# Optimization experiments

Hardware: AMD Instinct MI355X
Metric: run time of the kernel (lower is better)

Reference implementation:

```python
import jax, jax.numpy as jnp
import numpy as np

N_NODES = 100_000
N_EDGES = 1_600_000
N_GRAPHS = 64
EPS = 1e-7  # GENConv message epsilon
D_IN, D_H, D_OUT, OUT_DIM = 128, 192, 128, 10


def _w(k, fan_in, fan_out):
    return jax.random.normal(k, (fan_in, fan_out), jnp.float32) * (1.0 / np.sqrt(fan_in))


def setup_inputs() -> dict:
    key = jax.random.key(0)
    ks = jax.random.split(key, 8)
    return {
        "x": jax.random.normal(ks[0], (N_NODES, D_IN), jnp.float32),
        "W0": _w(ks[1], D_IN, D_H), "b0": jnp.zeros((D_H,), jnp.float32),
        "W1": _w(ks[2], D_H, D_H), "b1": jnp.zeros((D_H,), jnp.float32),
        "W2": _w(ks[3], D_H, D_H), "b2": jnp.zeros((D_H,), jnp.float32),
        "W3": _w(ks[4], D_H, D_OUT), "b3": jnp.zeros((D_OUT,), jnp.float32),
        "Wfc": _w(ks[5], D_OUT, OUT_DIM), "bfc": jnp.zeros((OUT_DIM,), jnp.float32),
        "edge_index": jax.random.randint(ks[6], (2, N_EDGES), 0, N_NODES, jnp.int32),
        "batch": jnp.sort(jax.random.randint(ks[7], (N_NODES,), 0, N_GRAPHS, jnp.int32)),
    }


def _genconv(x, W, b, src, dst):
    # GENConv (num_layers=1, aggr='add'): message = relu(x_j) + eps,
    # scatter-add to dst, residual add, single Linear MLP.
    msg = jax.nn.relu(x[src]) + EPS          # [E, d]
    agg = jax.ops.segment_sum(msg, dst, num_segments=N_NODES)  # [N, d]
    return (x + agg) @ W + b


def reference(x, W0, b0, W1, b1, W2, b2, W3, b3, Wfc, bfc, edge_index, batch):
    src, dst = edge_index[0], edge_index[1]  # source_to_target flow
    for W, b in ((W0, b0), (W1, b1), (W2, b2), (W3, b3)):
        x = _genconv(x, W, b, src, dst)
    # global mean pool over graphs
    sums = jax.ops.segment_sum(x, batch, num_segments=N_GRAPHS)
    counts = jax.ops.segment_sum(jnp.ones((x.shape[0],), x.dtype), batch,
                                 num_segments=N_GRAPHS)
    pooled = sums / jnp.maximum(counts, 1.0)[:, None]  # [G, D_OUT]
    logits = pooled @ Wfc + bfc                        # [G, OUT_DIM]
    return jax.nn.log_softmax(logits, axis=1)
```

## Files before the change

### kernel.cpp

```cpp
#include <hip/hip_runtime.h>
#include <hip/hip_bf16.h>
#include <stdint.h>

constexpr int NN = 100000;
constexpr int NE = 1600000;
constexpr int NG = 64;
constexpr int S  = 192;
constexpr int NB_SCAN = 98;
constexpr unsigned int ZOFF = (unsigned int)NN * 384u;

constexpr int PREP_INDEG_BLK = 1563;
constexpr int PREP_CONVX_BLK = 12500;
constexpr int PREP_CONVW_BLK = 384;
constexpr int PREP_GB_BLK    = 391;
constexpr int PREP_GRID = PREP_INDEG_BLK + PREP_CONVX_BLK + PREP_CONVW_BLK + PREP_GB_BLK;

constexpr int EG_BLOCKS = 391;
constexpr int HROW = 50048;
constexpr int QROW = HROW / 4;

typedef __bf16 bf16x8 __attribute__((ext_vector_type(8)));
typedef float  f32x16 __attribute__((ext_vector_type(16)));
typedef float  f32x2  __attribute__((ext_vector_type(2)));

union U16x4 { uint4 u; bf16x8 b; };

__device__ __forceinline__ float bl(unsigned int u) { return __uint_as_float(u << 16); }
__device__ __forceinline__ float bh(unsigned int u) { return __uint_as_float(u & 0xffff0000u); }
__device__ __forceinline__ float b16f(unsigned short u) { return __uint_as_float(((unsigned int)u) << 16); }
__device__ __forceinline__ unsigned int fb(float f) {
    unsigned int u = __float_as_uint(f);
    return (u + 0x7fffu + ((u >> 16) & 1u)) >> 16;
}
__device__ __forceinline__ unsigned int prelu(unsigned int u) {
    unsigned int r;
    asm("v_pk_max_f16 %0, %1, %2" : "=v"(r) : "v"(u), "v"(0u));
    return r;
}
__device__ __forceinline__ unsigned int cnt2bf(unsigned int h) {
    float f0 = (float)(h & 0xffffu);
    float f1 = (float)(h >> 16);
    return (__float_as_uint(f0) >> 16) | (__float_as_uint(f1) & 0xffff0000u);
}

__global__ __launch_bounds__(256) void k_prep(const float* __restrict__ x,
                                              const int* __restrict__ ei,
                                              const int* __restrict__ bat,
                                              const float* __restrict__ W0, const float* __restrict__ W1,
                                              const float* __restrict__ W2,
                                              unsigned short* __restrict__ A_,
                                              int* __restrict__ indeg, int* __restrict__ slot,
                                              unsigned short* __restrict__ T0, unsigned short* __restrict__ T1,
                                              unsigned short* __restrict__ T2,
                                              int* __restrict__ nstart) {
    const int b = blockIdx.x;
    if (b < PREP_INDEG_BLK) {
        int e4 = (b * 256 + threadIdx.x) * 4;
        if (e4 < NE) {
            int4 d = *(const int4*)(ei + NE + e4);
            int4 sl;
            sl.x = atomicAdd(&indeg[d.x], 1);
            sl.y = atomicAdd(&indeg[d.y], 1);
            sl.z = atomicAdd(&indeg[d.z], 1);
            sl.w = atomicAdd(&indeg[d.w], 1);
            *(int4*)(slot + e4) = sl;
        }
    } else if (b < PREP_INDEG_BLK + PREP_CONVX_BLK) {
        int id = (b - PREP_INDEG_BLK) * 256 + threadIdx.x;
        if (id < 96) ((unsigned int*)(A_ + (size_t)NN * S))[id] = 0u;
        int row = id >> 5, c4 = id & 31;
        float4 v = ((const float4*)x)[id];
        uint2 a;
        a.x = fb(v.x) | (fb(v.y) << 16);
        a.y = fb(v.z) | (fb(v.w) << 16);
        *(uint2*)(A_ + row * S + c4 * 4) = a;
    } else if (b < PREP_INDEG_BLK + PREP_CONVX_BLK + PREP_CONVW_BLK) {
        int id = (b - PREP_INDEG_BLK - PREP_CONVX_BLK) * 256 + threadIdx.x;
        const float* W; unsigned short* T; int N, base;
        if      (id < 24576) { W = W0; T = T0; N = 192; base = 0;     }
        else if (id < 61440) { W = W1; T = T1; N = 192; base = 24576; }
        else                 { W = W2; T = T2; N = 192; base = 61440; }
        int lid = id - base;
        int ci = lid >> 3, j = lid & 7;
        int kc = ci / N, n = ci % N;
        T[lid] = (unsigned short)fb(W[(kc * 8 + j) * N + n]);
    } else {
        int n = (b - PREP_INDEG_BLK - PREP_CONVX_BLK - PREP_CONVW_BLK) * 256 + threadIdx.x;
        if (n < NN) {
            int b0 = bat[n];
            int bprev = (n == 0) ? -1 : bat[n - 1];
            for (int g = bprev + 1; g <= b0; g++) nstart[g] = n;
            if (n == NN - 1)
                for (int g = b0 + 1; g < NG; g++) nstart[g] = NN;
        }
    }
}

__global__ __launch_bounds__(1024) void k_scan1(const int* __restrict__ indeg, int* __restrict__ offs,
                                                int* __restrict__ partials) {
    __shared__ int s[1024];
    int t = threadIdx.x;
    int gid = blockIdx.x * 1024 + t;
    int v = (gid < NN) ? indeg[gid] : 0;
    s[t] = v;
    __syncthreads();
    for (int d = 1; d < 1024; d <<= 1) {
        int tv = (t >= d) ? s[t - d] : 0;
        __syncthreads();
        s[t] += tv;
        __syncthreads();
    }
    if (gid < NN) offs[gid + 1] = s[t];
    if (t == 1023) partials[blockIdx.x] = s[1023];
}

__device__ __forceinline__ int toff(const int* __restrict__ offs, const int* __restrict__ part, int j) {
    return j ? (offs[j] + part[(j - 1) >> 10]) : 0;
}

__global__ __launch_bounds__(256) void k_fill(const int* __restrict__ ei, const int* __restrict__ offs,
                                              const int* __restrict__ praw,
                                              const int* __restrict__ slot, int* __restrict__ csr,
                                              int* __restrict__ part2) {
    __shared__ int s[128];
    __shared__ int spx[128];
    const int t = threadIdx.x;
    int v = 0;
    if (t < 128) {
        v = (t < NB_SCAN) ? praw[t] : 0;
        s[t] = v;
    }
    __syncthreads();
    for (int d = 1; d < 128; d <<= 1) {
        int tv = (t < 128 && t >= d) ? s[t - d] : 0;
        __syncthreads();
        if (t < 128) s[t] += tv;
        __syncthreads();
    }
    if (t < 128) spx[t] = s[t] - v;
    __syncthreads();
    if (blockIdx.x == 0 && t < NB_SCAN) part2[t] = spx[t];

    int e4 = (blockIdx.x * 256 + t) * 4;
    if (e4 >= NE) return;
    int4 sv = *(const int4*)(ei + e4);
    int4 dv = *(const int4*)(ei + NE + e4);
    int4 sl = *(const int4*)(slot + e4);
    csr[(dv.x ? offs[dv.x] + spx[(dv.x - 1) >> 10] : 0) + sl.x] = sv.x;
    csr[(dv.y ? offs[dv.y] + spx[(dv.y - 1) >> 10] : 0) + sl.y] = sv.y;
    csr[(dv.z ? offs[dv.z] + spx[(dv.z - 1) >> 10] : 0) + sl.z] = sv.z;
    csr[(dv.w ? offs[dv.w] + spx[(dv.w - 1) >> 10] : 0) + sl.w] = sv.w;
}

__global__ __launch_bounds__(256, 8) void k_agg192(const unsigned short* __restrict__ Ain,
                                                   unsigned short* __restrict__ Yout,
                                                   const int* __restrict__ offs,
                                                   const int* __restrict__ part,
                                                   const int* __restrict__ indeg,
                                                   const int* __restrict__ csr) {
    const int w = threadIdx.x >> 6, lane = threadIdx.x & 63;
    const int i = __builtin_amdgcn_readfirstlane(blockIdx.x * 4 + w);
    const bool act = lane < 48;
    const int deg   = __builtin_amdgcn_readfirstlane(indeg[i]);
    const int start = __builtin_amdgcn_readfirstlane(toff(offs, part, i));
    const int fo = (act ? lane : 47) * 8;
    const char* Ab = (const char*)Ain;

    f32x2 A01, A23;
    {
        uint2 p = *(const uint2*)(Ab + (size_t)i * 384 + fo);
        const float ed = 1e-7f * (float)deg;
        A01 = (f32x2){bl(p.x) + ed, bh(p.x) + ed};
        A23 = (f32x2){bl(p.y) + ed, bh(p.y) + ed};
    }

    const int* ecsr = csr + start;
    for (int e = 0; e < deg; e += 16) {
        unsigned int off[16];
#pragma unroll
        for (int k = 0; k < 16; k++) {
            int v = ecsr[e + k];
            off[k] = (e + k < deg) ? (unsigned int)v * 384u : ZOFF;
        }
        uint2 p[16];
#pragma unroll
        for (int k = 0; k < 16; k++)
            p[k] = *(const uint2*)(Ab + (size_t)off[k] + fo);
#pragma unroll
        for (int k = 0; k < 16; k++) {
            unsigned int rx = prelu(p[k].x), ry = prelu(p[k].y);
            A01 += (f32x2){bl(rx), bh(rx)};
            A23 += (f32x2){bl(ry), bh(ry)};
        }
    }
    if (act) {
        uint2 o;
        o.x = fb(A01.x) | (fb(A01.y) << 16);
        o.y = fb(A23.x) | (fb(A23.y) << 16);
        *(uint2*)(Yout + (size_t)i * S + lane * 4) = o;
    }
}

__global__ __launch_bounds__(256, 8) void k_agg128(const unsigned short* __restrict__ Ain,
                                                   unsigned short* __restrict__ Yout,
                                                   const int* __restrict__ offs,
                                                   const int* __restrict__ part,
                                                   const int* __restrict__ indeg,
                                                   const int* __restrict__ csr) {
    const int w = threadIdx.x >> 6, lane = threadIdx.x & 63;
    const int i = __builtin_amdgcn_readfirstlane(blockIdx.x * 4 + w);
    const int deg   = __builtin_amdgcn_readfirstlane(indeg[i]);
    const int start = __builtin_amdgcn_readfirstlane(toff(offs, part, i));
    const int fo = lane * 4;
    const char* Ab = (const char*)Ain;

    f32x2 A01;
    {
        unsigned int p = *(const unsigned int*)(Ab + (size_t)i * 384 + fo);
        const float ed = 1e-7f * (float)deg;
        A01 = (f32x2){bl(p) + ed, bh(p) + ed};
    }

    const int* ecsr = csr + start;
    for (int e = 0; e < deg; e += 16) {
        unsigned int off[16];
#pragma unroll
        for (int k = 0; k < 16; k++) {
            int v = ecsr[e + k];
            off[k] = (e + k < deg) ? (unsigned int)v * 384u : ZOFF;
        }
        unsigned int q[16];
#pragma unroll
        for (int k = 0; k < 16; k++)
            q[k] = *(const unsigned int*)(Ab + (size_t)off[k] + fo);
#pragma unroll
        for (int k = 0; k < 16; k++) {
            unsigned int r = prelu(q[k]);
            A01 += (f32x2){bl(r), bh(r)};
        }
    }
    *(unsigned int*)(Yout + (size_t)i * S + lane * 2) =
        fb(A01.x) | (fb(A01.y) << 16);
}

template <int K, int N>
__global__ __launch_bounds__(256) void k_gemm(const unsigned short* __restrict__ Yin,
                                              const unsigned short* __restrict__ WtC,
                                              const float* __restrict__ bias,
                                              unsigned short* __restrict__ Aout) {
    static_assert(K % 16 == 0 && N % 32 == 0, "");
    const int w = threadIdx.x >> 6, lane = threadIdx.x & 63;
    const int rt = blockIdx.x * 4 + w;
    if (rt >= (NN / 32)) return;
    const int hl = lane >> 5, lr = lane & 31;
    const int row0 = rt * 32;
    f32x16 acc[N / 32];
#pragma unroll
    for (int c = 0; c < N / 32; c++)
#pragma unroll
        for (int r = 0; r < 16; r++) acc[c][r] = 0.f;

    const unsigned short* ap = Yin + (row0 + lr) * S + hl * 8;
    const uint4* b4 = (const uint4*)WtC;
#pragma unroll
    for (int ks = 0; ks < K / 16; ks++) {
        U16x4 a;
        a.u = *(const uint4*)(ap + ks * 16);
#pragma unroll
        for (int c = 0; c < N / 32; c++) {
            U16x4 b;
            b.u = b4[(ks * 2 + hl) * N + c * 32 + lr];
            acc[c] = __builtin_amdgcn_mfma_f32_32x32x16_bf16(a.b, b.b, acc[c], 0, 0, 0);
        }
    }
#pragma unroll
    for (int c = 0; c < N / 32; c++) {
        const int col = c * 32 + lr;
        const float bc = bias[col];
#pragma unroll
        for (int r = 0; r < 16; r++) {
            const int row = row0 + (r & 3) + 8 * (r >> 2) + 4 * hl;
            Aout[row * S + col] = (unsigned short)fb(acc[c][r] + bc);
        }
    }
}

__global__ __launch_bounds__(256) void k_histpool(const int* __restrict__ csr,
                                                  const int* __restrict__ offs,
                                                  const int* __restrict__ part,
                                                  const int* __restrict__ nstart,
                                                  unsigned int* __restrict__ hist,
                                                  const unsigned short* __restrict__ X3,
                                                  const int* __restrict__ bat,
                                                  const int* __restrict__ indeg,
                                                  float* __restrict__ sums, float* __restrict__ cnt,
                                                  float* __restrict__ degsum) {
    const int b = blockIdx.x;
    if (b < 256) {
        const int g = b >> 2, q = b & 3;
        unsigned int* hrow = hist + (size_t)g * HROW;
        const unsigned int q0 = q * QROW;
        for (int i = threadIdx.x; i < QROW; i += 256) hrow[q0 + i] = 0u;
        __syncthreads();
        const int s0 = toff(offs, part, nstart[g]);
        const int s1 = (g == NG - 1) ? NE : toff(offs, part, nstart[g + 1]);
        for (int p = s0 + threadIdx.x; p < s1; p += 256) {
            int src = csr[p];
            unsigned int h = (unsigned int)src >> 1;
            if (h - q0 < (unsigned int)QROW)
                atomicAdd(&hrow[h], 1u << (16 * (src & 1)));
        }
    } else {
        const int pb = b - 256;
        const int f = threadIdx.x;
        if (f >= 192) return;
        int n0 = pb * 50;
        int n1 = min(n0 + 50, NN);
        int cur = bat[n0];
        float acc = 0.f;
        int run = 0, dacc = 0;
        for (int n = n0; n < n1; n++) {
            int g = bat[n];
            if (g != cur) {
                atomicAdd(&sums[cur * 192 + f], acc);
                if (f == 0) { atomicAdd(&cnt[cur], (float)run); atomicAdd(&degsum[cur], (float)dacc); }
                acc = 0.f; run = 0; dacc = 0; cur = g;
            }
            acc += b16f(X3[(size_t)n * S + f]);
            run++;
            if (f == 0) dacc += indeg[n];
        }
        atomicAdd(&sums[cur * 192 + f], acc);
        if (f == 0) { atomicAdd(&cnt[cur], (float)run); atomicAdd(&degsum[cur], (float)dacc); }
    }
}

__global__ __launch_bounds__(384) void k_egemm(const unsigned short* __restrict__ X3,
                                               const unsigned int* __restrict__ hist,
                                               float* __restrict__ partials) {
    const int wv = threadIdx.x >> 6, lane = threadIdx.x & 63;
    const int b = blockIdx.x;
    const int j0 = b * 256;
    const int hl = lane >> 5, lr = lane & 31;
    const int feat = wv * 32 + lr;
    f32x16 acc[2];
#pragma unroll
    for (int m = 0; m < 2; m++)
#pragma unroll
        for (int r = 0; r < 16; r++) acc[m][r] = 0.f;

    for (int kk = 0; kk < 16; kk++) {
        const int jh = (j0 >> 1) + kk * 8 + hl * 4;
        U16x4 af[2];
#pragma unroll
        for (int m = 0; m < 2; m++) {
            uint4 h = *(const uint4*)(hist + (size_t)(m * 32 + lr) * HROW + jh);
            af[m].u = (uint4){cnt2bf(h.x), cnt2bf(h.y), cnt2bf(h.z), cnt2bf(h.w)};
        }
        U16x4 bf;
#pragma unroll
        for (int tp = 0; tp < 4; tp++) {
            int je = j0 + kk * 16 + hl * 8 + tp * 2;
            int ja = min(je, NN), jb = min(je + 1, NN);
            unsigned int u0 = X3[(size_t)ja * S + feat];
            unsigned int u1 = X3[(size_t)jb * S + feat];
            ((unsigned int*)&bf.u)[tp] = prelu(u0 | (u1 << 16));
        }
#pragma unroll
        for (int m = 0; m < 2; m++)
            acc[m] = __builtin_amdgcn_mfma_f32_32x32x16_bf16(af[m].b, bf.b, acc[m], 0, 0, 0);
    }
    float* pb = partials + (size_t)b * 12288;
#pragma unroll
    for (int m = 0; m < 2; m++)
#pragma unroll
        for (int r = 0; r < 16; r++) {
            const int g = m * 32 + (r & 3) + 8 * (r >> 2) + 4 * hl;
            pb[g * 192 + feat] = acc[m][r];
        }
}

__global__ __launch_bounds__(192) void k_head(const float* __restrict__ sums,
                                              const float* __restrict__ partials,
                                              const float* __restrict__ cnt, const float* __restrict__ degsum,
                                              const float* __restrict__ W3, const float* __restrict__ b3,
                                              const float* __restrict__ Wfc, const float* __restrict__ bfc,
                                              float* __restrict__ out) {
    __shared__ float py[192];
    __shared__ float tl[128];
    __shared__ float lg[10];
    const int g = blockIdx.x, t = threadIdx.x;
    const float inv = 1.f / fmaxf(cnt[g], 1.f);
    const float ed = 1e-7f * degsum[g];
    const float* pp = partials + g * 192 + t;
    float s0 = 0.f, s1 = 0.f, s2 = 0.f, s3 = 0.f;
    int p = 0;
    for (; p + 4 <= EG_BLOCKS; p += 4) {
        s0 += pp[(size_t)(p + 0) * 12288];
        s1 += pp[(size_t)(p + 1) * 12288];
        s2 += pp[(size_t)(p + 2) * 12288];
        s3 += pp[(size_t)(p + 3) * 12288];
    }
    for (; p < EG_BLOCKS; p++) s0 += pp[(size_t)p * 12288];
    py[t] = (sums[g * 192 + t] + ((s0 + s1) + (s2 + s3)) + ed) * inv;
    __syncthreads();
    if (t < 128) {
        float tf = b3[t];
        for (int k = 0; k < 192; k++) tf += py[k] * W3[k * 128 + t];
        tl[t] = tf;
    }
    __syncthreads();
    if (t < 10) {
        float sf = bfc[t];
        for (int f = 0; f < 128; f++) sf += tl[f] * Wfc[f * 10 + t];
        lg[t] = sf;
    }
    __syncthreads();
    if (t < 10) {
        float m = lg[0];
        for (int k = 1; k < 10; k++) m = fmaxf(m, lg[k]);
        float se = 0.f;
        for (int k = 0; k < 10; k++) se += expf(lg[k] - m);
        out[g * 10 + t] = lg[t] - m - logf(se);
    }
}

constexpr size_t A0_OFF     = 0;
constexpr size_t A1_OFF     = 38400384;
constexpr size_t HIST_REL   = 0;
constexpr size_t PARTS_REL  = 12812288;
constexpr size_t CSR_OFF    = 76800384;
constexpr size_t OFFS_OFF   = 83200384;
constexpr size_t INDEG_OFF  = 83600512;
constexpr size_t SUMS_OFF   = 84000512;
constexpr size_t CNT_OFF    = 84049664;
constexpr size_t DEGS_OFF   = 84049920;
constexpr size_t PART_OFF   = 84050176;
constexpr size_t PART2_OFF  = 84050688;
constexpr size_t NSTART_OFF = 84051200;
constexpr size_t WT0_OFF    = 84051456;
constexpr size_t WT1_OFF    = 84100608;
constexpr size_t WT2_OFF    = 84174336;

extern "C" void kernel_launch(void* const* d_in, const int* in_sizes, int n_in,
                              void* d_out, int out_size, void* d_ws, size_t ws_size,
                              hipStream_t stream) {
    const float* x   = (const float*)d_in[0];
    const float* W0  = (const float*)d_in[1];
    const float* b0  = (const float*)d_in[2];
    const float* W1  = (const float*)d_in[3];
    const float* b1  = (const float*)d_in[4];
    const float* W2  = (const float*)d_in[5];
    const float* b2  = (const float*)d_in[6];
    const float* W3  = (const float*)d_in[7];
    const float* b3  = (const float*)d_in[8];
    const float* Wfc = (const float*)d_in[9];
    const float* bfc = (const float*)d_in[10];
    const int*   ei  = (const int*)d_in[11];
    const int*   bat = (const int*)d_in[12];
    float* out = (float*)d_out;

    char* ws = (char*)d_ws;
    unsigned short* A0  = (unsigned short*)(ws + A0_OFF);
    unsigned short* A1  = (unsigned short*)(ws + A1_OFF);
    int* slot   = (int*)(ws + A1_OFF);
    unsigned int* hist  = (unsigned int*)(ws + A1_OFF + HIST_REL);
    float* parts        = (float*)(ws + A1_OFF + PARTS_REL);
    int* csr    = (int*)(ws + CSR_OFF);
    int* offs   = (int*)(ws + OFFS_OFF);
    int* indeg  = (int*)(ws + INDEG_OFF);
    int* part   = (int*)(ws + PART_OFF);
    int* part2  = (int*)(ws + PART2_OFF);
    int* nstart = (int*)(ws + NSTART_OFF);
    unsigned short* Wt0 = (unsigned short*)(ws + WT0_OFF);
    unsigned short* Wt1 = (unsigned short*)(ws + WT1_OFF);
    unsigned short* Wt2 = (unsigned short*)(ws + WT2_OFF);
    float* sums   = (float*)(ws + SUMS_OFF);
    float* cnt    = (float*)(ws + CNT_OFF);
    float* degsum = (float*)(ws + DEGS_OFF);

    hipMemsetAsync(ws + INDEG_OFF, 0, 449664, stream);

    k_prep<<<PREP_GRID, 256, 0, stream>>>(x, ei, bat, W0, W1, W2, A0, indeg, slot,
                                          Wt0, Wt1, Wt2, nstart);

    k_scan1<<<NB_SCAN, 1024, 0, stream>>>(indeg, offs, part);
    k_fill<<<(NE / 4 + 255) / 256, 256, 0, stream>>>(ei, offs, part, slot, csr, part2);

    const int AGG_GRID  = NN / 4;
    const int GEMM_GRID = (NN / 32 + 3) / 4;

    k_agg128<<<AGG_GRID, 256, 0, stream>>>(A0, A1, offs, part2, indeg, csr);
    k_gemm<128, 192><<<GEMM_GRID, 256, 0, stream>>>(A1, Wt0, b0, A0);
    k_agg192<<<AGG_GRID, 256, 0, stream>>>(A0, A1, offs, part2, indeg, csr);
    k_gemm<192, 192><<<GEMM_GRID, 256, 0, stream>>>(A1, Wt1, b1, A0);
    k_agg192<<<AGG_GRID, 256, 0, stream>>>(A0, A1, offs, part2, indeg, csr);
    k_gemm<192, 192><<<GEMM_GRID, 256, 0, stream>>>(A1, Wt2, b2, A0);

    k_histpool<<<2256, 256, 0, stream>>>(csr, offs, part2, nstart, hist, A0, bat, indeg,
                                         sums, cnt, degsum);
    k_egemm<<<EG_BLOCKS, 384, 0, stream>>>(A0, hist, parts);
    k_head<<<NG, 192, 0, stream>>>(sums, parts, cnt, degsum, W3, b3, Wfc, bfc, out);
}
```

Baseline: 647.9 us.

## Split in-degree atomic counters into eight per-XCD copies to reduce contention

The in-degree counting atomics now go to eight separate counter arrays, one per block-index modulo 8, which on MI355X roughly maps to the XCD. This is meant to keep atomics local to one die's L2 and cut cross-die coherence traffic. The scan kernel merges the copies into a per-node total and a per-copy prefix, and the fill kernel adds that prefix when placing each CSR entry. In exchange it adds a larger memset, an extra prefix array and an extra gather in the fill, and it relies on the block-to-XCD mapping assumption for its locality benefit.

```diff
diff --git a/kernel.cpp b/kernel.cpp
--- a/kernel.cpp
+++ b/kernel.cpp
@@ -7,6 +7,7 @@
 constexpr int NG = 64;
 constexpr int S  = 192;
 constexpr int NB_SCAN = 98;
+constexpr int NN8 = 100352;
 constexpr unsigned int ZOFF = (unsigned int)NN * 384u;
 
 constexpr int PREP_INDEG_BLK = 1563;
@@ -49,7 +50,7 @@
                                               const float* __restrict__ W0, const float* __restrict__ W1,
                                               const float* __restrict__ W2,
                                               unsigned short* __restrict__ A_,
-                                              int* __restrict__ indeg, int* __restrict__ slot,
+                                              int* __restrict__ indeg8, int* __restrict__ slot,
                                               unsigned short* __restrict__ T0, unsigned short* __restrict__ T1,
                                               unsigned short* __restrict__ T2,
                                               int* __restrict__ nstart) {
@@ -57,12 +58,13 @@
     if (b < PREP_INDEG_BLK) {
         int e4 = (b * 256 + threadIdx.x) * 4;
         if (e4 < NE) {
+            int* cp = indeg8 + (b & 7) * NN8;
             int4 d = *(const int4*)(ei + NE + e4);
             int4 sl;
-            sl.x = atomicAdd(&indeg[d.x], 1);
-            sl.y = atomicAdd(&indeg[d.y], 1);
-            sl.z = atomicAdd(&indeg[d.z], 1);
-            sl.w = atomicAdd(&indeg[d.w], 1);
+            sl.x = atomicAdd(&cp[d.x], 1);
+            sl.y = atomicAdd(&cp[d.y], 1);
+            sl.z = atomicAdd(&cp[d.z], 1);
+            sl.w = atomicAdd(&cp[d.w], 1);
             *(int4*)(slot + e4) = sl;
         }
     } else if (b < PREP_INDEG_BLK + PREP_CONVX_BLK) {
@@ -96,12 +98,30 @@
     }
 }
 
-__global__ __launch_bounds__(1024) void k_scan1(const int* __restrict__ indeg, int* __restrict__ offs,
-                                                int* __restrict__ partials) {
+__global__ __launch_bounds__(1024) void k_scan1(const int* __restrict__ indeg8,
+                                                int* __restrict__ indeg,
+                                                unsigned short* __restrict__ pxcd,
+                                                int* __restrict__ offs,
+                                                int* __restrict__ partials,
+                                                float* __restrict__ zero_region) {
     __shared__ int s[1024];
     int t = threadIdx.x;
     int gid = blockIdx.x * 1024 + t;
-    int v = (gid < NN) ? indeg[gid] : 0;
+    int v = 0;
+    if (gid < NN) {
+        int run = 0;
+#pragma unroll
+        for (int x = 0; x < 8; x++) {
+            int c = indeg8[x * NN8 + gid];
+            pxcd[x * NN8 + gid] = (unsigned short)run;
+            run += c;
+        }
+        v = run;
+        indeg[gid] = run;
+    }
+    if (blockIdx.x == 0) {
+        for (int i = t; i < 12416; i += 1024) zero_region[i] = 0.f;
+    }
     s[t] = v;
     __syncthreads();
     for (int d = 1; d < 1024; d <<= 1) {
@@ -120,7 +140,9 @@
 
 __global__ __launch_bounds__(256) void k_fill(const int* __restrict__ ei, const int* __restrict__ offs,
                                               const int* __restrict__ praw,
-                                              const int* __restrict__ slot, int* __restrict__ csr,
+                                              const int* __restrict__ slot,
+                                              const unsigned short* __restrict__ pxcd,
+                                              int* __restrict__ csr,
                                               int* __restrict__ part2) {
     __shared__ int s[128];
     __shared__ int spx[128];
@@ -143,13 +165,14 @@
 
     int e4 = (blockIdx.x * 256 + t) * 4;
     if (e4 >= NE) return;
+    const unsigned short* px = pxcd + (size_t)((e4 >> 10) & 7) * NN8;
     int4 sv = *(const int4*)(ei + e4);
     int4 dv = *(const int4*)(ei + NE + e4);
     int4 sl = *(const int4*)(slot + e4);
-    csr[(dv.x ? offs[dv.x] + spx[(dv.x - 1) >> 10] : 0) + sl.x] = sv.x;
-    csr[(dv.y ? offs[dv.y] + spx[(dv.y - 1) >> 10] : 0) + sl.y] = sv.y;
-    csr[(dv.z ? offs[dv.z] + spx[(dv.z - 1) >> 10] : 0) + sl.z] = sv.z;
-    csr[(dv.w ? offs[dv.w] + spx[(dv.w - 1) >> 10] : 0) + sl.w] = sv.w;
+    csr[(dv.x ? offs[dv.x] + spx[(dv.x - 1) >> 10] : 0) + px[dv.x] + sl.x] = sv.x;
+    csr[(dv.y ? offs[dv.y] + spx[(dv.y - 1) >> 10] : 0) + px[dv.y] + sl.y] = sv.y;
+    csr[(dv.z ? offs[dv.z] + spx[(dv.z - 1) >> 10] : 0) + px[dv.z] + sl.z] = sv.z;
+    csr[(dv.w ? offs[dv.w] + spx[(dv.w - 1) >> 10] : 0) + px[dv.w] + sl.w] = sv.w;
 }
 
 __global__ __launch_bounds__(256, 8) void k_agg192(const unsigned short* __restrict__ Ain,
@@ -425,22 +448,25 @@
     }
 }
 
-constexpr size_t A0_OFF     = 0;
-constexpr size_t A1_OFF     = 38400384;
-constexpr size_t HIST_REL   = 0;
-constexpr size_t PARTS_REL  = 12812288;
-constexpr size_t CSR_OFF    = 76800384;
-constexpr size_t OFFS_OFF   = 83200384;
-constexpr size_t INDEG_OFF  = 83600512;
-constexpr size_t SUMS_OFF   = 84000512;
-constexpr size_t CNT_OFF    = 84049664;
-constexpr size_t DEGS_OFF   = 84049920;
-constexpr size_t PART_OFF   = 84050176;
-constexpr size_t PART2_OFF  = 84050688;
-constexpr size_t NSTART_OFF = 84051200;
-constexpr size_t WT0_OFF    = 84051456;
-constexpr size_t WT1_OFF    = 84100608;
-constexpr size_t WT2_OFF    = 84174336;
+constexpr size_t A0_OFF      = 0;
+constexpr size_t A1_OFF      = 38400384;
+constexpr size_t SLOT_REL    = 0;
+constexpr size_t INDEG8_REL  = 6400000;
+constexpr size_t PXCD_REL    = 9611264;
+constexpr size_t HIST_REL    = 0;
+constexpr size_t PARTS_REL   = 12812288;
+constexpr size_t CSR_OFF     = 76800768;
+constexpr size_t OFFS_OFF    = 83200768;
+constexpr size_t INDEG_OFF   = 83600896;
+constexpr size_t SUMS_OFF    = 84000896;
+constexpr size_t CNT_OFF     = 84050048;
+constexpr size_t DEGS_OFF    = 84050304;
+constexpr size_t PART_OFF    = 84050560;
+constexpr size_t PART2_OFF   = 84051072;
+constexpr size_t NSTART_OFF  = 84051584;
+constexpr size_t WT0_OFF     = 84051840;
+constexpr size_t WT1_OFF     = 84100992;
+constexpr size_t WT2_OFF     = 84174720;
 
 extern "C" void kernel_launch(void* const* d_in, const int* in_sizes, int n_in,
                               void* d_out, int out_size, void* d_ws, size_t ws_size,
@@ -463,9 +489,11 @@
     char* ws = (char*)d_ws;
     unsigned short* A0  = (unsigned short*)(ws + A0_OFF);
     unsigned short* A1  = (unsigned short*)(ws + A1_OFF);
-    int* slot   = (int*)(ws + A1_OFF);
-    unsigned int* hist  = (unsigned int*)(ws + A1_OFF + HIST_REL);
-    float* parts        = (float*)(ws + A1_OFF + PARTS_REL);
+    int* slot            = (int*)(ws + A1_OFF + SLOT_REL);
+    int* indeg8          = (int*)(ws + A1_OFF + INDEG8_REL);
+    unsigned short* pxcd = (unsigned short*)(ws + A1_OFF + PXCD_REL);
+    unsigned int* hist   = (unsigned int*)(ws + A1_OFF + HIST_REL);
+    float* parts         = (float*)(ws + A1_OFF + PARTS_REL);
     int* csr    = (int*)(ws + CSR_OFF);
     int* offs   = (int*)(ws + OFFS_OFF);
     int* indeg  = (int*)(ws + INDEG_OFF);
@@ -479,13 +507,13 @@
     float* cnt    = (float*)(ws + CNT_OFF);
     float* degsum = (float*)(ws + DEGS_OFF);
 
-    hipMemsetAsync(ws + INDEG_OFF, 0, 449664, stream);
-
-    k_prep<<<PREP_GRID, 256, 0, stream>>>(x, ei, bat, W0, W1, W2, A0, indeg, slot,
+    hipMemsetAsync(ws + A1_OFF + INDEG8_REL, 0, 3211264, stream);
+
+    k_prep<<<PREP_GRID, 256, 0, stream>>>(x, ei, bat, W0, W1, W2, A0, indeg8, slot,
                                           Wt0, Wt1, Wt2, nstart);
 
-    k_scan1<<<NB_SCAN, 1024, 0, stream>>>(indeg, offs, part);
-    k_fill<<<(NE / 4 + 255) / 256, 256, 0, stream>>>(ei, offs, part, slot, csr, part2);
+    k_scan1<<<NB_SCAN, 1024, 0, stream>>>(indeg8, indeg, pxcd, offs, part, sums);
+    k_fill<<<(NE / 4 + 255) / 256, 256, 0, stream>>>(ei, offs, part, slot, pxcd, csr, part2);
 
     const int AGG_GRID  = NN / 4;
     const int GEMM_GRID = (NN / 32 + 3) / 4;
```

Result: no change. 649.1 us (+0.2%).
